# Kernel optimization log

Hardware: AMD Instinct MI355X
Metric: run time of the kernel (lower is better)

Reference implementation:

```python
import jax, jax.numpy as jnp
import numpy as np

B, N, D, H = 256, 1000, 128, 8
DH = D // H
TANH_CLIP = 10.0
NEG = -1e9  # finite stand-in for -inf mask fill (keeps grads clean)


def setup_inputs() -> dict:
    key = jax.random.key(0)
    ks = jax.random.split(key, 8)
    s = 1.0 / np.sqrt(D)
    return {
        "node_embeddings": jax.random.normal(ks[0], (B, N, D), jnp.float32),
        "W_node": jax.random.normal(ks[1], (D, 3 * D), jnp.float32) * s,   # project_node_embeddings
        "W_fixed": jax.random.normal(ks[2], (D, D), jnp.float32) * s,      # project_fixed_context
        "W_step": jax.random.normal(ks[3], (2 * D, D), jnp.float32) * s,   # project_step_context
        "W_out": jax.random.normal(ks[4], (D, D), jnp.float32) * s,        # project_out
        "prev_idx": jax.random.randint(ks[5], (B,), 0, N),
        "first_idx": jax.random.randint(ks[6], (B,), 0, N),
        "mask": jax.random.randint(ks[7], (B, N), 0, 2).astype(bool),      # True = masked/visited
    }


def reference(node_embeddings, W_node, W_fixed, W_step, W_out, prev_idx, first_idx, mask):
    b = jnp.arange(B)
    # Precompute fixed: context projection of graph embedding (mean aggregation)
    graph_embed = node_embeddings.mean(axis=1)                    # (B, D)
    fixed_context = graph_embed @ W_fixed                          # (B, D)
    # glimpse key / glimpse val / logit key from node embeddings
    kvl = node_embeddings @ W_node                                 # (B, N, 3D)
    glimpse_K, glimpse_V, logit_K = jnp.split(kvl, 3, axis=-1)
    gK = glimpse_K.reshape(B, N, H, DH)                            # (B, N, H, dh)
    gV = glimpse_V.reshape(B, N, H, DH)
    # Step context: cat(first node embed, last node embed) -> query
    step_ctx = jnp.concatenate(
        [node_embeddings[b, first_idx], node_embeddings[b, prev_idx]], axis=-1)  # (B, 2D)
    query = fixed_context + step_ctx @ W_step                      # (B, D)
    Q = query.reshape(B, H, DH)                                    # (B, H, dh)
    # Glimpse MHA (single query per batch element)
    compat = jnp.einsum("bhd,bnhd->bhn", Q, gK) / np.sqrt(DH)      # (B, H, N)
    compat = jnp.where(mask[:, None, :], NEG, compat)              # mask_inner
    attn = jax.nn.softmax(compat, axis=-1)
    heads = jnp.einsum("bhn,bnhd->bhd", attn, gV)                  # (B, H, dh)
    glimpse = heads.reshape(B, D) @ W_out                          # (B, D)
    # Logits against logit_K, tanh clipping, mask_logits, log-softmax
    logits = jnp.einsum("bd,bnd->bn", glimpse, logit_K) / np.sqrt(D)
    logits = TANH_CLIP * jnp.tanh(logits)
    logits = jnp.where(mask, NEG, logits)
    log_p = jax.nn.log_softmax(logits, axis=-1)                    # (B, N)
    return log_p
```

## Files before the change

kernel.cpp:

```cpp
#include <hip/hip_runtime.h>
#include <math.h>

#define BB 256
#define NN 1000
#define DD 128
#define HH 8
#define QQ 4
#define RQ 250
#define NEG -1e9f

#define SY_CNTA 0
#define SY_CNTC 1
#define SY_CNTE 2

__device__ __forceinline__ bool get_mask(const void* m, int flag, size_t idx) {
    if (flag == 1) return ((const int*)m)[idx] != 0;
    if (flag == 2) return ((const float*)m)[idx] != 0.0f;
    return ((const unsigned char*)m)[idx] != 0;
}

__device__ __forceinline__ void sy_barrier(int* p, int tid, int tgt) {
    if (tid == 0) {
        __builtin_amdgcn_fence(__ATOMIC_RELEASE, "agent");
        __hip_atomic_fetch_add(p, 1, __ATOMIC_RELAXED, __HIP_MEMORY_SCOPE_AGENT);
        while (__hip_atomic_load(p, __ATOMIC_RELAXED, __HIP_MEMORY_SCOPE_AGENT) < tgt)
            __builtin_amdgcn_s_sleep(8);
        __builtin_amdgcn_fence(__ATOMIC_ACQUIRE, "agent");
    }
    __syncthreads();
}

__global__ __launch_bounds__(256, 4) void k_one(
        const float* __restrict__ X, const float* __restrict__ Wnode,
        const float* __restrict__ Wfix, const float* __restrict__ Wstep,
        const float* __restrict__ Wout, const int* __restrict__ prev,
        const int* __restrict__ first, const void* __restrict__ mask,
        int* __restrict__ syg, float* __restrict__ partial,
        float* __restrict__ sqw, float* __restrict__ pvp,
        float* __restrict__ esumg, float* __restrict__ out) {
    const int bid = blockIdx.x, tid = threadIdx.x;
    const int b = bid >> 2, q = bid & 3;
    const int n0 = q * RQ;
    const size_t xoff = (size_t)b * NN * DD;
    int* sy = syg + b * 16;

    __shared__ __align__(16) float pool[4096];
    __shared__ __align__(16) float qks[HH][DD];
    __shared__ float gqv[DD];
    __shared__ float lgl[256];
    __shared__ unsigned short cidxL[256];
    __shared__ float redS[4][HH];
    __shared__ float Sh[HH];
    __shared__ float redw[4];
    __shared__ int wbase[4];
    __shared__ int s_flag, s_cnt;

    if (tid < 64) {
        const unsigned int* mw = (const unsigned int*)mask;
        unsigned int a0 = mw[tid], a1 = mw[tid + 64], a2 = mw[tid + 128], a3 = mw[tid + 192];
        int ii = (a0 <= 1u) && (a1 <= 1u) && (a2 <= 1u) && (a3 <= 1u);
        int ff = (a0 == 0u || a0 == 0x3F800000u) && (a1 == 0u || a1 == 0x3F800000u) &&
                 (a2 == 0u || a2 == 0x3F800000u) && (a3 == 0u || a3 == 0x3F800000u);
        int ai = __all(ii), af = __all(ff);
        if (tid == 0) s_flag = ai ? 1 : (af ? 2 : 0);
    }

    {
        float4* red4 = (float4*)pool;
        int c = tid & 31, s = tid >> 5;
        const float4* Xr = (const float4*)(X + xoff);
        float4 acc = make_float4(0.f, 0.f, 0.f, 0.f);
        for (int nl = s; nl < RQ; nl += 8) {
            float4 v = Xr[(n0 + nl) * 32 + c];
            acc.x += v.x; acc.y += v.y; acc.z += v.z; acc.w += v.w;
        }
        red4[s * 32 + c] = acc;
        __syncthreads();
        for (int st = 4; st >= 1; st >>= 1) {
            if (s < st) {
                float4 o = red4[(s + st) * 32 + c];
                float4 r = red4[s * 32 + c];
                r.x += o.x; r.y += o.y; r.z += o.z; r.w += o.w;
                red4[s * 32 + c] = r;
            }
            __syncthreads();
        }
        if (s == 0) {
            float4 r = red4[c];
            float* outp = partial + ((size_t)b * QQ + q) * DD + 4 * c;
            outp[0] = r.x; outp[1] = r.y; outp[2] = r.z; outp[3] = r.w;
        }
    }
    {
        int w = tid >> 6, lane = tid & 63;
        bool un = (tid < RQ) && !get_mask(mask, s_flag, (size_t)b * NN + n0 + tid);
        unsigned long long bal = __ballot(un);
        if (lane == 0) wbase[w] = __popcll(bal);
        __syncthreads();
        int base = 0;
        for (int ww = 0; ww < w; ++ww) base += wbase[ww];
        int off = __popcll(bal & ((1ULL << lane) - 1ULL));
        if (un) cidxL[base + off] = (unsigned short)tid;
        if (tid == 0) s_cnt = wbase[0] + wbase[1] + wbase[2] + wbase[3];
    }
    __syncthreads();
    sy_barrier(&sy[SY_CNTA], tid, QQ);

    {
        float* ge = pool;
        float* sc = pool + 128;
        float* qv = pool + 384;
        float* qp = pool + 512;
        if (tid < DD) {
            float g = 0.f;
            #pragma unroll
            for (int qq = 0; qq < QQ; ++qq) g += partial[((size_t)b * QQ + qq) * DD + tid];
            ge[tid] = g * (1.0f / NN);
        }
        {
            int src = (tid < DD) ? first[b] : prev[b];
            sc[tid] = X[xoff + (size_t)src * DD + (tid & 127)];
        }
        __syncthreads();
        int p = tid >> 7, d = tid & 127;
        {
            float a = 0.f;
            #pragma unroll 8
            for (int k = p * 64; k < p * 64 + 64; ++k)      a += ge[k] * Wfix[(size_t)k * DD + d];
            #pragma unroll 8
            for (int k = p * 128; k < p * 128 + 128; ++k)   a += sc[k] * Wstep[(size_t)k * DD + d];
            qp[p * DD + d] = a;
        }
        __syncthreads();
        if (tid < DD) qv[tid] = qp[tid] + qp[DD + tid];
        __syncthreads();
        {
            const float* wrow = Wnode + (size_t)d * 384;
            #pragma unroll
            for (int h = p * 4; h < p * 4 + 4; ++h) {
                const float4* wr = (const float4*)(wrow + h * 16);
                float a = 0.f;
                #pragma unroll
                for (int j4 = 0; j4 < 4; ++j4) {
                    float4 w = wr[j4];
                    a += w.x * qv[h * 16 + 4 * j4]     + w.y * qv[h * 16 + 4 * j4 + 1]
                       + w.z * qv[h * 16 + 4 * j4 + 2] + w.w * qv[h * 16 + 4 * j4 + 3];
                }
                qks[h][d] = 0.25f * a;
            }
        }
        __syncthreads();
    }

    {
        float* redpv = pool;
        const int lane = tid & 63, w = tid >> 6;
        const int h = lane & 7, cg = lane >> 3;
        const int len = s_cnt;
        const int iters = (len + 3) >> 2;

        float4 qk0, qk1, qk2, qk3;
        {
            const float4* qr = (const float4*)&qks[h][cg * 16];
            qk0 = qr[0]; qk1 = qr[1]; qk2 = qr[2]; qk3 = qr[3];
        }
        float acc[16];
        #pragma unroll
        for (int j = 0; j < 16; ++j) acc[j] = 0.f;
        float S = 0.f;

        float4 v0, v1, v2, v3;
        if (iters > 0) {
            int kk = (w < len) ? w : (len - 1);
            int n = n0 + cidxL[kk];
            const float4* xr = (const float4*)(X + xoff + (size_t)n * DD + cg * 16);
            v0 = xr[0]; v1 = xr[1]; v2 = xr[2]; v3 = xr[3];
        }
        for (int it = 0; it < iters; ++it) {
            int k = it * 4 + w;
            bool valid = (k < len);
            float4 p0 = v0, p1 = v1, p2 = v2, p3 = v3;
            if (it + 1 < iters) {
                int kn = k + 4;
                int kk = (kn < len) ? kn : (len - 1);
                int n = n0 + cidxL[kk];
                const float4* xr = (const float4*)(X + xoff + (size_t)n * DD + cg * 16);
                p0 = xr[0]; p1 = xr[1]; p2 = xr[2]; p3 = xr[3];
            }
            float cp = v0.x * qk0.x + v0.y * qk0.y + v0.z * qk0.z + v0.w * qk0.w
                     + v1.x * qk1.x + v1.y * qk1.y + v1.z * qk1.z + v1.w * qk1.w
                     + v2.x * qk2.x + v2.y * qk2.y + v2.z * qk2.z + v2.w * qk2.w
                     + v3.x * qk3.x + v3.y * qk3.y + v3.z * qk3.z + v3.w * qk3.w;
            cp += __shfl_xor(cp, 8, 64);
            cp += __shfl_xor(cp, 16, 64);
            cp += __shfl_xor(cp, 32, 64);
            float pe = valid ? __expf(fminf(cp, 80.f)) : 0.f;
            S += pe;
            acc[0]  += pe * v0.x; acc[1]  += pe * v0.y; acc[2]  += pe * v0.z; acc[3]  += pe * v0.w;
            acc[4]  += pe * v1.x; acc[5]  += pe * v1.y; acc[6]  += pe * v1.z; acc[7]  += pe * v1.w;
            acc[8]  += pe * v2.x; acc[9]  += pe * v2.y; acc[10] += pe * v2.z; acc[11] += pe * v2.w;
            acc[12] += pe * v3.x; acc[13] += pe * v3.y; acc[14] += pe * v3.z; acc[15] += pe * v3.w;
            v0 = p0; v1 = p1; v2 = p2; v3 = p3;
        }
        {
            float* dst = &redpv[((size_t)w * HH + h) * DD + cg * 16];
            *((float4*)&dst[0])  = make_float4(acc[0],  acc[1],  acc[2],  acc[3]);
            *((float4*)&dst[4])  = make_float4(acc[4],  acc[5],  acc[6],  acc[7]);
            *((float4*)&dst[8])  = make_float4(acc[8],  acc[9],  acc[10], acc[11]);
            *((float4*)&dst[12]) = make_float4(acc[12], acc[13], acc[14], acc[15]);
            if (lane < 8) redS[w][lane] = S;
        }
        __syncthreads();
        for (int idx = tid; idx < HH * DD; idx += 256) {
            int hh = idx >> 7, d = idx & 127;
            pvp[(((size_t)b * QQ + q) * HH + hh) * DD + d] =
                redpv[(0 * HH + hh) * DD + d] + redpv[(1 * HH + hh) * DD + d] +
                redpv[(2 * HH + hh) * DD + d] + redpv[(3 * HH + hh) * DD + d];
        }
        if (tid < HH)
            sqw[((size_t)b * QQ + q) * HH + tid] =
                redS[0][tid] + redS[1][tid] + redS[2][tid] + redS[3][tid];
    }
    __syncthreads();
    sy_barrier(&sy[SY_CNTC], tid, QQ);

    {
        float* xa = pool;
        float* hd = pool + 1024;
        float* gl = pool + 1152;
        float* qp = pool + 1280;
        if (tid < HH) {
            float S = 0.f;
            #pragma unroll
            for (int qq = 0; qq < QQ; ++qq) S += sqw[((size_t)b * QQ + qq) * HH + tid];
            Sh[tid] = 1.0f / S;
        }
        if (tid < RQ) lgl[tid] = NEG;
        __syncthreads();
        for (int idx = tid; idx < HH * DD; idx += 256) {
            int h = idx >> 7, d = idx & 127;
            float a = 0.f;
            #pragma unroll
            for (int qq = 0; qq < QQ; ++qq)
                a += pvp[(((size_t)b * QQ + qq) * HH + h) * DD + d];
            xa[h * DD + d] = a * Sh[h];
        }
        __syncthreads();
        int p = tid >> 7, t = tid & 127;
        {
            int h = t >> 4;
            float a = 0.f;
            #pragma unroll 8
            for (int d = p * 64; d < p * 64 + 64; ++d)
                a += xa[h * DD + d] * Wnode[(size_t)d * 384 + 128 + t];
            qp[p * DD + t] = a;
        }
        __syncthreads();
        if (tid < DD) hd[tid] = qp[tid] + qp[DD + tid];
        __syncthreads();
        {
            float a = 0.f;
            #pragma unroll 8
            for (int k = p * 64; k < p * 64 + 64; ++k) a += hd[k] * Wout[(size_t)k * DD + t];
            qp[p * DD + t] = a;
        }
        __syncthreads();
        if (tid < DD) gl[tid] = qp[tid] + qp[DD + tid];
        __syncthreads();
        {
            const float4* wr = (const float4*)(Wnode + (size_t)t * 384 + 256 + p * 64);
            float a = 0.f;
            #pragma unroll
            for (int j4 = 0; j4 < 16; ++j4) {
                float4 w = wr[j4];
                int k = p * 64 + 4 * j4;
                a += w.x * gl[k] + w.y * gl[k + 1] + w.z * gl[k + 2] + w.w * gl[k + 3];
            }
            qp[p * DD + t] = a;
        }
        __syncthreads();
        if (tid < DD) gqv[tid] = (qp[tid] + qp[DD + tid]) * 0.08838834764831845f;
        __syncthreads();
    }

    {
        const int len = s_cnt;
        const int iters = (len + 31) >> 5;
        int g = tid & 7, rr = tid >> 3;
        float esum = 0.f;
        for (int it = 0; it < iters; ++it) {
            int k = it * 32 + rr;
            bool valid = (k < len);
            int kk = valid ? k : (len - 1);
            int nl = cidxL[kk];
            const float4* xr = (const float4*)(X + xoff + (size_t)(n0 + nl) * DD);
            float a = 0.f;
            #pragma unroll
            for (int i = 0; i < 4; ++i) {
                float4 v = xr[g + 8 * i];
                int col = 4 * (g + 8 * i);
                a += v.x * gqv[col] + v.y * gqv[col + 1]
                   + v.z * gqv[col + 2] + v.w * gqv[col + 3];
            }
            a += __shfl_xor(a, 1, 8);
            a += __shfl_xor(a, 2, 8);
            a += __shfl_xor(a, 4, 8);
            if (g == 0 && valid) {
                float l = 10.0f * tanhf(a);
                lgl[nl] = l;
                esum += __expf(l - 10.0f);
            }
        }
        #pragma unroll
        for (int off = 32; off >= 1; off >>= 1) esum += __shfl_xor(esum, off, 64);
        if ((tid & 63) == 0) redw[tid >> 6] = esum;
        __syncthreads();
        if (tid == 0) esumg[(size_t)b * QQ + q] = redw[0] + redw[1] + redw[2] + redw[3];
    }
    __syncthreads();
    sy_barrier(&sy[SY_CNTE], tid, QQ);

    {
        float s = esumg[(size_t)b * QQ] + esumg[(size_t)b * QQ + 1]
                + esumg[(size_t)b * QQ + 2] + esumg[(size_t)b * QQ + 3];
        float lse = 10.0f + logf(s);
        if (tid < RQ) out[(size_t)b * NN + n0 + tid] = lgl[tid] - lse;
    }
}

__global__ __launch_bounds__(1024) void k_mega(
        const float* __restrict__ X, const float* __restrict__ Wnode,
        const float* __restrict__ Wfix, const float* __restrict__ Wstep,
        const float* __restrict__ Wout, const int* __restrict__ prev,
        const int* __restrict__ first, const void* __restrict__ mask,
        float* __restrict__ out) {
    int b = blockIdx.x, tid = threadIdx.x;
    __shared__ __align__(16) float cm[HH * 1024];
    __shared__ __align__(16) float qkl[HH * DD];
    __shared__ __align__(16) float qpart[8 * DD];
    __shared__ float xa[HH * DD];
    __shared__ float ge[DD], q[DD], sc[2 * DD], hd[DD], gl[DD], gqv[DD];
    __shared__ float red[16], invh[8];
    __shared__ int s_flag;
    const size_t xoff = (size_t)b * NN * DD;

    if (tid < 64) {
        const unsigned int* mw = (const unsigned int*)mask;
        unsigned int a0 = mw[tid], a1 = mw[tid + 64], a2 = mw[tid + 128], a3 = mw[tid + 192];
        int ii = (a0 <= 1u) && (a1 <= 1u) && (a2 <= 1u) && (a3 <= 1u);
        int ff = (a0 == 0u || a0 == 0x3F800000u) && (a1 == 0u || a1 == 0x3F800000u) &&
                 (a2 == 0u || a2 == 0x3F800000u) && (a3 == 0u || a3 == 0x3F800000u);
        int ai = __all(ii), af = __all(ff);
        if (tid == 0) s_flag = ai ? 1 : (af ? 2 : 0);
    }
    if (tid >= 256 && tid < 512) {
        int t = tid - 256;
        int src = (t < DD) ? first[b] : prev[b];
        sc[t] = X[xoff + (size_t)src * DD + (t & 127)];
    }
    {
        float4* red4 = (float4*)cm;
        int c = tid & 31, s = tid >> 5;
        const float4* Xr = (const float4*)(X + xoff);
        float4 acc = make_float4(0.f, 0.f, 0.f, 0.f);
        for (int n = s; n < NN; n += 32) {
            float4 v = Xr[n * 32 + c];
            acc.x += v.x; acc.y += v.y; acc.z += v.z; acc.w += v.w;
        }
        red4[s * 32 + c] = acc;
        __syncthreads();
        for (int st = 16; st >= 1; st >>= 1) {
            if (s < st) {
                float4 o = red4[(s + st) * 32 + c];
                float4 r = red4[s * 32 + c];
                r.x += o.x; r.y += o.y; r.z += o.z; r.w += o.w;
                red4[s * 32 + c] = r;
            }
            __syncthreads();
        }
        if (s == 0) {
            float4 r = red4[c];
            ge[4 * c] = r.x * (1.0f / NN); ge[4 * c + 1] = r.y * (1.0f / NN);
            ge[4 * c + 2] = r.z * (1.0f / NN); ge[4 * c + 3] = r.w * (1.0f / NN);
        }
        __syncthreads();
    }
    const int flag = s_flag;
    {
        int p = tid >> 7, d = tid & 127;
        float a = 0.f;
        for (int k = p * 16; k < p * 16 + 16; ++k) a += ge[k] * Wfix[k * DD + d];
        for (int k = p * 32; k < p * 32 + 32; ++k) a += sc[k] * Wstep[k * DD + d];
        qpart[p * DD + d] = a;
        __syncthreads();
        if (tid < DD) {
            float s = 0.f;
            for (int pp = 0; pp < 8; ++pp) s += qpart[pp * DD + tid];
            q[tid] = s;
        }
        __syncthreads();
        int d2 = tid >> 3, h = tid & 7;
        const float4* wr = (const float4*)(Wnode + (size_t)d2 * 384 + h * 16);
        float a2 = 0.f;
        for (int j4 = 0; j4 < 4; ++j4) {
            float4 w = wr[j4];
            a2 += w.x * q[h * 16 + 4 * j4]     + w.y * q[h * 16 + 4 * j4 + 1]
                + w.z * q[h * 16 + 4 * j4 + 2] + w.w * q[h * 16 + 4 * j4 + 3];
        }
        qkl[h * DD + d2] = 0.25f * a2;
        __syncthreads();
    }
    {
        int g = tid & 7;
        for (int it = 0; it < 8; ++it) {
            int n = it * 128 + (tid >> 3);
            if (n < NN) {
                float acc[HH] = {0.f, 0.f, 0.f, 0.f, 0.f, 0.f, 0.f, 0.f};
                const float4* xr = (const float4*)(X + xoff + (size_t)n * DD);
                for (int i = 0; i < 4; ++i) {
                    float4 v = xr[g + 8 * i];
                    int col = 4 * (g + 8 * i);
                    for (int h = 0; h < HH; ++h)
                        acc[h] += v.x * qkl[h * DD + col]     + v.y * qkl[h * DD + col + 1]
                                + v.z * qkl[h * DD + col + 2] + v.w * qkl[h * DD + col + 3];
                }
                for (int h = 0; h < HH; ++h) {
                    acc[h] += __shfl_xor(acc[h], 1, 8);
                    acc[h] += __shfl_xor(acc[h], 2, 8);
                    acc[h] += __shfl_xor(acc[h], 4, 8);
                }
                float val = acc[0];
                for (int h = 1; h < HH; ++h) val = (g == h) ? acc[h] : val;
                bool mk = get_mask(mask, flag, (size_t)b * NN + n);
                cm[g * 1024 + n] = mk ? NEG : val;
            }
        }
        __syncthreads();
    }
    {
        int h = tid >> 7, lane = tid & 127;
        float mx = -INFINITY;
        for (int n = lane; n < NN; n += 128) mx = fmaxf(mx, cm[h * 1024 + n]);
        for (int off = 32; off >= 1; off >>= 1) mx = fmaxf(mx, __shfl_xor(mx, off, 64));
        if ((tid & 63) == 0) red[tid >> 6] = mx;
        __syncthreads();
        float m_h = fmaxf(red[2 * h], red[2 * h + 1]);
        float sm = 0.f;
        for (int n = lane; n < NN; n += 128) {
            float p = __expf(cm[h * 1024 + n] - m_h);
            cm[h * 1024 + n] = p;
            sm += p;
        }
        for (int off = 32; off >= 1; off >>= 1) sm += __shfl_xor(sm, off, 64);
        __syncthreads();
        if ((tid & 63) == 0) red[tid >> 6] = sm;
        __syncthreads();
        if (tid < HH) invh[tid] = 1.0f / (red[2 * tid] + red[2 * tid + 1]);
        __syncthreads();
    }
    {
        int s = tid >> 7, d = tid & 127;
        float acc[HH] = {0.f, 0.f, 0.f, 0.f, 0.f, 0.f, 0.f, 0.f};
        for (int n = s; n < NN; n += 8) {
            float x = X[xoff + (size_t)n * DD + d];
            for (int h = 0; h < HH; ++h) acc[h] += cm[h * 1024 + n] * x;
        }
        __syncthreads();
        float* xp = cm;
        for (int h = 0; h < HH; ++h) xp[(s * HH + h) * DD + d] = acc[h];
        __syncthreads();
        if (s == 0) {
            for (int h = 0; h < HH; ++h) {
                float t = 0.f;
                for (int ss = 0; ss < 8; ++ss) t += xp[(ss * HH + h) * DD + d];
                xa[h * DD + d] = t * invh[h];
            }
        }
        __syncthreads();
    }
    {
        int p = tid >> 7, t = tid & 127;
        int h = t >> 4;
        float a = 0.f;
        for (int d = p * 16; d < p * 16 + 16; ++d)
            a += xa[h * DD + d] * Wnode[(size_t)d * 384 + 128 + t];
        qpart[p * DD + t] = a;
        __syncthreads();
        if (tid < DD) {
            float s = 0.f;
            for (int pp = 0; pp < 8; ++pp) s += qpart[pp * DD + tid];
            hd[tid] = s;
        }
        __syncthreads();
        a = 0.f;
        for (int k = p * 16; k < p * 16 + 16; ++k) a += hd[k] * Wout[(size_t)k * DD + t];
        qpart[p * DD + t] = a;
        __syncthreads();
        if (tid < DD) {
            float s = 0.f;
            for (int pp = 0; pp < 8; ++pp) s += qpart[pp * DD + tid];
            gl[tid] = s;
        }
        __syncthreads();
        const float4* wr = (const float4*)(Wnode + (size_t)t * 384 + 256 + p * 16);
        a = 0.f;
        for (int j4 = 0; j4 < 4; ++j4) {
            float4 w = wr[j4];
            int k = p * 16 + 4 * j4;
            a += w.x * gl[k] + w.y * gl[k + 1] + w.z * gl[k + 2] + w.w * gl[k + 3];
        }
        qpart[p * DD + t] = a;
        __syncthreads();
        if (tid < DD) {
            float s = 0.f;
            for (int pp = 0; pp < 8; ++pp) s += qpart[pp * DD + tid];
            gqv[tid] = s * 0.08838834764831845f;
        }
        __syncthreads();
    }
    {
        float* lg = qkl;
        int g = tid & 7;
        for (int it = 0; it < 8; ++it) {
            int n = it * 128 + (tid >> 3);
            if (n < NN) {
                const float4* xr = (const float4*)(X + xoff + (size_t)n * DD);
                float a = 0.f;
                for (int i = 0; i < 4; ++i) {
                    float4 v = xr[g + 8 * i];
                    int col = 4 * (g + 8 * i);
                    a += v.x * gqv[col] + v.y * gqv[col + 1] + v.z * gqv[col + 2] + v.w * gqv[col + 3];
                }
                a += __shfl_xor(a, 1, 8);
                a += __shfl_xor(a, 2, 8);
                a += __shfl_xor(a, 4, 8);
                if (g == 0) {
                    float lgt = 10.0f * tanhf(a);
                    lg[n] = get_mask(mask, flag, (size_t)b * NN + n) ? NEG : lgt;
                }
            }
        }
        __syncthreads();
        float v = (tid < NN) ? lg[tid] : -INFINITY;
        float mx = v;
        for (int off = 32; off >= 1; off >>= 1) mx = fmaxf(mx, __shfl_xor(mx, off, 64));
        if ((tid & 63) == 0) red[tid >> 6] = mx;
        __syncthreads();
        float m = red[0];
        for (int w = 1; w < 16; ++w) m = fmaxf(m, red[w]);
        float e = (tid < NN) ? __expf(v - m) : 0.f;
        float sm = e;
        for (int off = 32; off >= 1; off >>= 1) sm += __shfl_xor(sm, off, 64);
        __syncthreads();
        if ((tid & 63) == 0) red[tid >> 6] = sm;
        __syncthreads();
        float s2 = 0.f;
        for (int w = 0; w < 16; ++w) s2 += red[w];
        float lse = m + logf(s2);
        if (tid < NN) out[(size_t)b * NN + tid] = v - lse;
    }
}

extern "C" void kernel_launch(void* const* d_in, const int* in_sizes, int n_in,
                              void* d_out, int out_size, void* d_ws, size_t ws_size,
                              hipStream_t stream) {
    const float* X     = (const float*)d_in[0];
    const float* Wnode = (const float*)d_in[1];
    const float* Wfix  = (const float*)d_in[2];
    const float* Wstep = (const float*)d_in[3];
    const float* Wout  = (const float*)d_in[4];
    const int*   prev  = (const int*)d_in[5];
    const int*   first = (const int*)d_in[6];
    const void*  mask  = d_in[7];
    float* out = (float*)d_out;

    char* wsb = (char*)d_ws;
    int*   syg     = (int*)wsb;
    float* partial = (float*)(wsb + 16384);
    float* sqw     = partial + (size_t)BB * QQ * DD;
    float* pvp     = sqw + (size_t)BB * QQ * HH;
    float* esumg   = pvp + (size_t)BB * QQ * HH * DD;
    const size_t need = 16384 + sizeof(float) * (
        (size_t)BB * QQ * DD + (size_t)BB * QQ * HH +
        (size_t)BB * QQ * HH * DD + (size_t)BB * QQ);

    int maxb = 0;
    bool ok = (ws_size >= need) &&
              (hipOccupancyMaxActiveBlocksPerMultiprocessor(&maxb, (const void*)k_one,
                                                            256, 0) == hipSuccess) &&
              (maxb >= QQ);
    if (ok) {
        hipMemsetAsync(syg, 0, 16384, stream);
        k_one<<<BB * QQ, 256, 0, stream>>>(X, Wnode, Wfix, Wstep, Wout, prev, first,
                                           mask, syg, partial, sqw, pvp, esumg, out);
    } else {
        k_mega<<<BB, 1024, 0, stream>>>(X, Wnode, Wfix, Wstep, Wout,
                                        prev, first, mask, out);
    }
}
```

Baseline: 107.4 us.

## Split each batch row across 8 cooperating blocks with leader-computed shared projections

Templates the cooperative kernel on the chunk count and launches 8 blocks per batch row instead of 4, falling back to 4 and then the monolithic kernel when occupancy is insufficient. The small per-row projections (query-key and glimpse-query vectors) are now computed once by the chunk-0 block and published through global memory with flag signals, instead of every block redundantly computing them. Per-wave partial attention results are written straight to global memory rather than reduced in shared memory first, and the register prefetch of the next row is dropped. This aims to raise parallelism and cut redundant work, at the cost of serializing followers on the leader block and more global traffic and spin-waiting.

```diff
diff --git a/kernel.cpp b/kernel.cpp
--- a/kernel.cpp
+++ b/kernel.cpp
@@ -5,13 +5,13 @@
 #define NN 1000
 #define DD 128
 #define HH 8
-#define QQ 4
-#define RQ 250
 #define NEG -1e9f
 
 #define SY_CNTA 0
-#define SY_CNTC 1
-#define SY_CNTE 2
+#define SY_QK   1
+#define SY_CNTC 2
+#define SY_GQ   3
+#define SY_CNTE 4
 
 __device__ __forceinline__ bool get_mask(const void* m, int flag, size_t idx) {
     if (flag == 1) return ((const int*)m)[idx] != 0;
@@ -19,37 +19,42 @@
     return ((const unsigned char*)m)[idx] != 0;
 }
 
-__device__ __forceinline__ void sy_barrier(int* p, int tid, int tgt) {
-    if (tid == 0) {
-        __builtin_amdgcn_fence(__ATOMIC_RELEASE, "agent");
-        __hip_atomic_fetch_add(p, 1, __ATOMIC_RELAXED, __HIP_MEMORY_SCOPE_AGENT);
-        while (__hip_atomic_load(p, __ATOMIC_RELAXED, __HIP_MEMORY_SCOPE_AGENT) < tgt)
-            __builtin_amdgcn_s_sleep(8);
-        __builtin_amdgcn_fence(__ATOMIC_ACQUIRE, "agent");
-    }
-    __syncthreads();
+__device__ __forceinline__ void sy_arrive(int* p) {
+    __builtin_amdgcn_fence(__ATOMIC_RELEASE, "agent");
+    __hip_atomic_fetch_add(p, 1, __ATOMIC_RELAXED, __HIP_MEMORY_SCOPE_AGENT);
 }
-
-__global__ __launch_bounds__(256, 4) void k_one(
+__device__ __forceinline__ void sy_set(int* p) {
+    __builtin_amdgcn_fence(__ATOMIC_RELEASE, "agent");
+    __hip_atomic_store(p, 1, __ATOMIC_RELAXED, __HIP_MEMORY_SCOPE_AGENT);
+}
+__device__ __forceinline__ void sy_wait(int* p, int tgt) {
+    while (__hip_atomic_load(p, __ATOMIC_RELAXED, __HIP_MEMORY_SCOPE_AGENT) < tgt)
+        __builtin_amdgcn_s_sleep(8);
+    __builtin_amdgcn_fence(__ATOMIC_ACQUIRE, "agent");
+}
+
+template<int CC>
+__global__ __launch_bounds__(256, CC) void k_one(
         const float* __restrict__ X, const float* __restrict__ Wnode,
         const float* __restrict__ Wfix, const float* __restrict__ Wstep,
         const float* __restrict__ Wout, const int* __restrict__ prev,
         const int* __restrict__ first, const void* __restrict__ mask,
         int* __restrict__ syg, float* __restrict__ partial,
-        float* __restrict__ sqw, float* __restrict__ pvp,
+        float* __restrict__ qkg, float* __restrict__ sqw,
+        float* __restrict__ pvp, float* __restrict__ gqg,
         float* __restrict__ esumg, float* __restrict__ out) {
+    const int RC = NN / CC;
     const int bid = blockIdx.x, tid = threadIdx.x;
-    const int b = bid >> 2, q = bid & 3;
-    const int n0 = q * RQ;
+    const int b = bid / CC, ch = bid % CC;
+    const int n0 = ch * RC;
     const size_t xoff = (size_t)b * NN * DD;
     int* sy = syg + b * 16;
 
-    __shared__ __align__(16) float pool[4096];
-    __shared__ __align__(16) float qks[HH][DD];
+    __shared__ __align__(16) float pool[1536];
+    __shared__ __align__(16) float qks[HH * DD];
     __shared__ float gqv[DD];
     __shared__ float lgl[256];
     __shared__ unsigned short cidxL[256];
-    __shared__ float redS[4][HH];
     __shared__ float Sh[HH];
     __shared__ float redw[4];
     __shared__ int wbase[4];
@@ -70,7 +75,7 @@
         int c = tid & 31, s = tid >> 5;
         const float4* Xr = (const float4*)(X + xoff);
         float4 acc = make_float4(0.f, 0.f, 0.f, 0.f);
-        for (int nl = s; nl < RQ; nl += 8) {
+        for (int nl = s; nl < RC; nl += 8) {
             float4 v = Xr[(n0 + nl) * 32 + c];
             acc.x += v.x; acc.y += v.y; acc.z += v.z; acc.w += v.w;
         }
@@ -87,13 +92,13 @@
         }
         if (s == 0) {
             float4 r = red4[c];
-            float* outp = partial + ((size_t)b * QQ + q) * DD + 4 * c;
+            float* outp = partial + ((size_t)b * CC + ch) * DD + 4 * c;
             outp[0] = r.x; outp[1] = r.y; outp[2] = r.z; outp[3] = r.w;
         }
     }
     {
         int w = tid >> 6, lane = tid & 63;
-        bool un = (tid < RQ) && !get_mask(mask, s_flag, (size_t)b * NN + n0 + tid);
+        bool un = (tid < RC) && !get_mask(mask, s_flag, (size_t)b * NN + n0 + tid);
         unsigned long long bal = __ballot(un);
         if (lane == 0) wbase[w] = __popcll(bal);
         __syncthreads();
@@ -104,9 +109,11 @@
         if (tid == 0) s_cnt = wbase[0] + wbase[1] + wbase[2] + wbase[3];
     }
     __syncthreads();
-    sy_barrier(&sy[SY_CNTA], tid, QQ);
-
-    {
+    if (tid == 0) sy_arrive(&sy[SY_CNTA]);
+
+    if (ch == 0) {
+        if (tid == 0) sy_wait(&sy[SY_CNTA], CC);
+        __syncthreads();
         float* ge = pool;
         float* sc = pool + 128;
         float* qv = pool + 384;
@@ -114,7 +121,7 @@
         if (tid < DD) {
             float g = 0.f;
             #pragma unroll
-            for (int qq = 0; qq < QQ; ++qq) g += partial[((size_t)b * QQ + qq) * DD + tid];
+            for (int cc = 0; cc < CC; ++cc) g += partial[((size_t)b * CC + cc) * DD + tid];
             ge[tid] = g * (1.0f / NN);
         }
         {
@@ -125,9 +132,9 @@
         int p = tid >> 7, d = tid & 127;
         {
             float a = 0.f;
-            #pragma unroll 8
+            #pragma unroll 4
             for (int k = p * 64; k < p * 64 + 64; ++k)      a += ge[k] * Wfix[(size_t)k * DD + d];
-            #pragma unroll 8
+            #pragma unroll 4
             for (int k = p * 128; k < p * 128 + 128; ++k)   a += sc[k] * Wstep[(size_t)k * DD + d];
             qp[p * DD + d] = a;
         }
@@ -146,14 +153,18 @@
                     a += w.x * qv[h * 16 + 4 * j4]     + w.y * qv[h * 16 + 4 * j4 + 1]
                        + w.z * qv[h * 16 + 4 * j4 + 2] + w.w * qv[h * 16 + 4 * j4 + 3];
                 }
-                qks[h][d] = 0.25f * a;
-            }
-        }
-        __syncthreads();
-    }
-
-    {
-        float* redpv = pool;
+                qkg[((size_t)b * HH + h) * DD + d] = 0.25f * a;
+            }
+        }
+        __syncthreads();
+        if (tid == 0) sy_set(&sy[SY_QK]);
+    }
+    if (tid == 0) sy_wait(&sy[SY_QK], 1);
+    __syncthreads();
+    for (int i = tid; i < HH * DD; i += 256) qks[i] = qkg[(size_t)b * HH * DD + i];
+    __syncthreads();
+
+    {
         const int lane = tid & 63, w = tid >> 6;
         const int h = lane & 7, cg = lane >> 3;
         const int len = s_cnt;
@@ -161,7 +172,7 @@
 
         float4 qk0, qk1, qk2, qk3;
         {
-            const float4* qr = (const float4*)&qks[h][cg * 16];
+            const float4* qr = (const float4*)&qks[h * DD + cg * 16];
             qk0 = qr[0]; qk1 = qr[1]; qk2 = qr[2]; qk3 = qr[3];
         }
         float acc[16];
@@ -169,24 +180,13 @@
         for (int j = 0; j < 16; ++j) acc[j] = 0.f;
         float S = 0.f;
 
-        float4 v0, v1, v2, v3;
-        if (iters > 0) {
-            int kk = (w < len) ? w : (len - 1);
-            int n = n0 + cidxL[kk];
-            const float4* xr = (const float4*)(X + xoff + (size_t)n * DD + cg * 16);
-            v0 = xr[0]; v1 = xr[1]; v2 = xr[2]; v3 = xr[3];
-        }
         for (int it = 0; it < iters; ++it) {
             int k = it * 4 + w;
             bool valid = (k < len);
-            float4 p0 = v0, p1 = v1, p2 = v2, p3 = v3;
-            if (it + 1 < iters) {
-                int kn = k + 4;
-                int kk = (kn < len) ? kn : (len - 1);
-                int n = n0 + cidxL[kk];
-                const float4* xr = (const float4*)(X + xoff + (size_t)n * DD + cg * 16);
-                p0 = xr[0]; p1 = xr[1]; p2 = xr[2]; p3 = xr[3];
-            }
+            int kk = valid ? k : 0;
+            int n = n0 + cidxL[kk];
+            const float4* xr = (const float4*)(X + xoff + (size_t)n * DD + cg * 16);
+            float4 v0 = xr[0], v1 = xr[1], v2 = xr[2], v3 = xr[3];
             float cp = v0.x * qk0.x + v0.y * qk0.y + v0.z * qk0.z + v0.w * qk0.w
                      + v1.x * qk1.x + v1.y * qk1.y + v1.z * qk1.z + v1.w * qk1.w
                      + v2.x * qk2.x + v2.y * qk2.y + v2.z * qk2.z + v2.w * qk2.w
@@ -200,57 +200,44 @@
             acc[4]  += pe * v1.x; acc[5]  += pe * v1.y; acc[6]  += pe * v1.z; acc[7]  += pe * v1.w;
             acc[8]  += pe * v2.x; acc[9]  += pe * v2.y; acc[10] += pe * v2.z; acc[11] += pe * v2.w;
             acc[12] += pe * v3.x; acc[13] += pe * v3.y; acc[14] += pe * v3.z; acc[15] += pe * v3.w;
-            v0 = p0; v1 = p1; v2 = p2; v3 = p3;
-        }
-        {
-            float* dst = &redpv[((size_t)w * HH + h) * DD + cg * 16];
-            *((float4*)&dst[0])  = make_float4(acc[0],  acc[1],  acc[2],  acc[3]);
-            *((float4*)&dst[4])  = make_float4(acc[4],  acc[5],  acc[6],  acc[7]);
-            *((float4*)&dst[8])  = make_float4(acc[8],  acc[9],  acc[10], acc[11]);
-            *((float4*)&dst[12]) = make_float4(acc[12], acc[13], acc[14], acc[15]);
-            if (lane < 8) redS[w][lane] = S;
-        }
-        __syncthreads();
-        for (int idx = tid; idx < HH * DD; idx += 256) {
-            int hh = idx >> 7, d = idx & 127;
-            pvp[(((size_t)b * QQ + q) * HH + hh) * DD + d] =
-                redpv[(0 * HH + hh) * DD + d] + redpv[(1 * HH + hh) * DD + d] +
-                redpv[(2 * HH + hh) * DD + d] + redpv[(3 * HH + hh) * DD + d];
-        }
-        if (tid < HH)
-            sqw[((size_t)b * QQ + q) * HH + tid] =
-                redS[0][tid] + redS[1][tid] + redS[2][tid] + redS[3][tid];
-    }
-    __syncthreads();
-    sy_barrier(&sy[SY_CNTC], tid, QQ);
-
-    {
+        }
+        const size_t slot = ((size_t)b * CC + ch) * 4 + w;
+        float* dst = pvp + slot * (HH * DD) + h * DD + cg * 16;
+        *((float4*)&dst[0])  = make_float4(acc[0],  acc[1],  acc[2],  acc[3]);
+        *((float4*)&dst[4])  = make_float4(acc[4],  acc[5],  acc[6],  acc[7]);
+        *((float4*)&dst[8])  = make_float4(acc[8],  acc[9],  acc[10], acc[11]);
+        *((float4*)&dst[12]) = make_float4(acc[12], acc[13], acc[14], acc[15]);
+        if (lane < 8) sqw[slot * HH + lane] = S;
+    }
+    __syncthreads();
+    if (tid == 0) sy_arrive(&sy[SY_CNTC]);
+
+    if (ch == 0) {
+        if (tid == 0) sy_wait(&sy[SY_CNTC], CC);
+        __syncthreads();
         float* xa = pool;
         float* hd = pool + 1024;
         float* gl = pool + 1152;
         float* qp = pool + 1280;
         if (tid < HH) {
             float S = 0.f;
-            #pragma unroll
-            for (int qq = 0; qq < QQ; ++qq) S += sqw[((size_t)b * QQ + qq) * HH + tid];
+            for (int s = 0; s < CC * 4; ++s)
+                S += sqw[((size_t)b * CC * 4 + s) * HH + tid];
             Sh[tid] = 1.0f / S;
         }
-        if (tid < RQ) lgl[tid] = NEG;
         __syncthreads();
         for (int idx = tid; idx < HH * DD; idx += 256) {
-            int h = idx >> 7, d = idx & 127;
             float a = 0.f;
-            #pragma unroll
-            for (int qq = 0; qq < QQ; ++qq)
-                a += pvp[(((size_t)b * QQ + qq) * HH + h) * DD + d];
-            xa[h * DD + d] = a * Sh[h];
+            for (int s = 0; s < CC * 4; ++s)
+                a += pvp[((size_t)b * CC * 4 + s) * (HH * DD) + idx];
+            xa[idx] = a * Sh[idx >> 7];
         }
         __syncthreads();
         int p = tid >> 7, t = tid & 127;
         {
             int h = t >> 4;
             float a = 0.f;
-            #pragma unroll 8
+            #pragma unroll 4
             for (int d = p * 64; d < p * 64 + 64; ++d)
                 a += xa[h * DD + d] * Wnode[(size_t)d * 384 + 128 + t];
             qp[p * DD + t] = a;
@@ -260,7 +247,7 @@
         __syncthreads();
         {
             float a = 0.f;
-            #pragma unroll 8
+            #pragma unroll 4
             for (int k = p * 64; k < p * 64 + 64; ++k) a += hd[k] * Wout[(size_t)k * DD + t];
             qp[p * DD + t] = a;
         }
@@ -270,7 +257,7 @@
         {
             const float4* wr = (const float4*)(Wnode + (size_t)t * 384 + 256 + p * 64);
             float a = 0.f;
-            #pragma unroll
+            #pragma unroll 4
             for (int j4 = 0; j4 < 16; ++j4) {
                 float4 w = wr[j4];
                 int k = p * 64 + 4 * j4;
@@ -279,9 +266,16 @@
             qp[p * DD + t] = a;
         }
         __syncthreads();
-        if (tid < DD) gqv[tid] = (qp[tid] + qp[DD + tid]) * 0.08838834764831845f;
-        __syncthreads();
-    }
+        if (tid < DD)
+            gqg[(size_t)b * DD + tid] = (qp[tid] + qp[DD + tid]) * 0.08838834764831845f;
+        __syncthreads();
+        if (tid == 0) sy_set(&sy[SY_GQ]);
+    }
+    if (tid == 0) sy_wait(&sy[SY_GQ], 1);
+    __syncthreads();
+    if (tid < DD) gqv[tid] = gqg[(size_t)b * DD + tid];
+    for (int i = tid; i < RC; i += 256) lgl[i] = NEG;
+    __syncthreads();
 
     {
         const int len = s_cnt;
@@ -291,7 +285,7 @@
         for (int it = 0; it < iters; ++it) {
             int k = it * 32 + rr;
             bool valid = (k < len);
-            int kk = valid ? k : (len - 1);
+            int kk = valid ? k : 0;
             int nl = cidxL[kk];
             const float4* xr = (const float4*)(X + xoff + (size_t)(n0 + nl) * DD);
             float a = 0.f;
@@ -315,16 +309,18 @@
         for (int off = 32; off >= 1; off >>= 1) esum += __shfl_xor(esum, off, 64);
         if ((tid & 63) == 0) redw[tid >> 6] = esum;
         __syncthreads();
-        if (tid == 0) esumg[(size_t)b * QQ + q] = redw[0] + redw[1] + redw[2] + redw[3];
-    }
-    __syncthreads();
-    sy_barrier(&sy[SY_CNTE], tid, QQ);
-
-    {
-        float s = esumg[(size_t)b * QQ] + esumg[(size_t)b * QQ + 1]
-                + esumg[(size_t)b * QQ + 2] + esumg[(size_t)b * QQ + 3];
+        if (tid == 0) esumg[(size_t)b * CC + ch] = redw[0] + redw[1] + redw[2] + redw[3];
+    }
+    __syncthreads();
+    if (tid == 0) { sy_arrive(&sy[SY_CNTE]); sy_wait(&sy[SY_CNTE], CC); }
+    __syncthreads();
+
+    {
+        float s = 0.f;
+        for (int cc = 0; cc < CC; ++cc) s += esumg[(size_t)b * CC + cc];
         float lse = 10.0f + logf(s);
-        if (tid < RQ) out[(size_t)b * NN + n0 + tid] = lgl[tid] - lse;
+        for (int i = tid; i < RC; i += 256)
+            out[(size_t)b * NN + n0 + i] = lgl[i] - lse;
     }
 }
 
@@ -577,22 +573,31 @@
     char* wsb = (char*)d_ws;
     int*   syg     = (int*)wsb;
     float* partial = (float*)(wsb + 16384);
-    float* sqw     = partial + (size_t)BB * QQ * DD;
-    float* pvp     = sqw + (size_t)BB * QQ * HH;
-    float* esumg   = pvp + (size_t)BB * QQ * HH * DD;
+    float* qkg     = partial + (size_t)BB * 8 * DD;
+    float* sqw     = qkg + (size_t)BB * HH * DD;
+    float* pvp     = sqw + (size_t)BB * 8 * 4 * HH;
+    float* gqg     = pvp + (size_t)BB * 8 * 4 * HH * DD;
+    float* esumg   = gqg + (size_t)BB * DD;
     const size_t need = 16384 + sizeof(float) * (
-        (size_t)BB * QQ * DD + (size_t)BB * QQ * HH +
-        (size_t)BB * QQ * HH * DD + (size_t)BB * QQ);
-
-    int maxb = 0;
-    bool ok = (ws_size >= need) &&
-              (hipOccupancyMaxActiveBlocksPerMultiprocessor(&maxb, (const void*)k_one,
-                                                            256, 0) == hipSuccess) &&
-              (maxb >= QQ);
-    if (ok) {
+        (size_t)BB * 8 * DD + (size_t)BB * HH * DD + (size_t)BB * 8 * 4 * HH +
+        (size_t)BB * 8 * 4 * HH * DD + (size_t)BB * DD + (size_t)BB * 8);
+
+    int maxb8 = 0, maxb4 = 0;
+    bool ws_ok = (ws_size >= need);
+    if (ws_ok) {
+        hipOccupancyMaxActiveBlocksPerMultiprocessor(&maxb8, (const void*)k_one<8>, 256, 0);
+        hipOccupancyMaxActiveBlocksPerMultiprocessor(&maxb4, (const void*)k_one<4>, 256, 0);
+    }
+    if (ws_ok && maxb8 >= 8) {
         hipMemsetAsync(syg, 0, 16384, stream);
-        k_one<<<BB * QQ, 256, 0, stream>>>(X, Wnode, Wfix, Wstep, Wout, prev, first,
-                                           mask, syg, partial, sqw, pvp, esumg, out);
+        k_one<8><<<BB * 8, 256, 0, stream>>>(X, Wnode, Wfix, Wstep, Wout, prev, first,
+                                             mask, syg, partial, qkg, sqw, pvp, gqg,
+                                             esumg, out);
+    } else if (ws_ok && maxb4 >= 4) {
+        hipMemsetAsync(syg, 0, 16384, stream);
+        k_one<4><<<BB * 4, 256, 0, stream>>>(X, Wnode, Wfix, Wstep, Wout, prev, first,
+                                             mask, syg, partial, qkg, sqw, pvp, gqg,
+                                             esumg, out);
     } else {
         k_mega<<<BB, 1024, 0, stream>>>(X, Wnode, Wfix, Wstep, Wout,
                                         prev, first, mask, out);
```

After: 107.5 us. No clear change (+0.1%).
